# Performance work log

Measured on AMD Instinct MI355X. Metric: run time of the kernel, lower is better.

## Reference

```python
import jax, jax.numpy as jnp
import numpy as np

N = 384      # max_nodes
H = 256      # layers[0] == layers[1] == layers[2]
Z = 128      # dim_z
ED = 128     # edge_dim
AH = ED // 2 # attention hidden

# complete directed graph: combinations (i<j) then reversed pairs
_i, _j = np.triu_indices(N, k=1)
_SRC = jnp.asarray(np.concatenate([_i, _j]), dtype=jnp.int32)  # edge_index[0]
_DST = jnp.asarray(np.concatenate([_j, _i]), dtype=jnp.int32)  # edge_index[1]


def setup_inputs() -> dict:
    key = jax.random.key(0)
    ks = jax.random.split(key, 16)
    def p(k, shape, fan_in):
        return jax.random.normal(k, shape, dtype=jnp.float32) * (1.0 / np.sqrt(fan_in))
    return {
        "z": jax.random.normal(ks[0], (1, Z), dtype=jnp.float32),
        # GRU (torch layout: W_ih [3H, Z], W_hh [3H, H]; gate order r, z, n)
        "gru_Wih": p(ks[1], (3 * H, Z), Z),
        "gru_Whh": p(ks[2], (3 * H, H), H),
        "gru_bih": jnp.zeros((3 * H,), jnp.float32),
        "gru_bhh": jnp.zeros((3 * H,), jnp.float32),
        # edge_generator MLP: 2H -> 4H -> ED
        "eg_W1": p(ks[3], (2 * H, 4 * H), 2 * H), "eg_b1": jnp.zeros((4 * H,), jnp.float32),
        "eg_W2": p(ks[4], (4 * H, ED), 4 * H),   "eg_b2": jnp.zeros((ED,), jnp.float32),
        # attention MLPs: (ED+H) -> ED//2 -> 1
        "att0_W1": p(ks[5], (ED + H, AH), ED + H), "att0_b1": jnp.zeros((AH,), jnp.float32),
        "att0_W2": p(ks[6], (AH, 1), AH),           "att0_b2": jnp.zeros((1,), jnp.float32),
        "att1_W1": p(ks[7], (ED + H, AH), ED + H), "att1_b1": jnp.zeros((AH,), jnp.float32),
        "att1_W2": p(ks[8], (AH, 1), AH),           "att1_b2": jnp.zeros((1,), jnp.float32),
        # EdgeConv output linears: H -> H
        "conv0_W": p(ks[9], (H, H), H),  "conv0_b": jnp.zeros((H,), jnp.float32),
        "conv1_W": p(ks[10], (H, H), H), "conv1_b": jnp.zeros((H,), jnp.float32),
    }


def _forward(z, gru_Wih, gru_Whh, gru_bih, gru_bhh,
             eg_W1, eg_b1, eg_W2, eg_b2,
             att0_W1, att0_b1, att0_W2, att0_b2,
             att1_W1, att1_b1, att1_W2, att1_b2,
             conv0_W, conv0_b, conv1_W, conv1_b):
    # --- GRU node generation: input is the same latent z at every step ---
    gi = z[0] @ gru_Wih.T + gru_bih            # [3H], constant per step
    gir, giz, gin = jnp.split(gi, 3)
    def step(h, _):
        gh = h @ gru_Whh.T + gru_bhh
        ghr, ghz, ghn = jnp.split(gh, 3)
        r = jax.nn.sigmoid(gir + ghr)
        u = jax.nn.sigmoid(giz + ghz)
        n = jnp.tanh(gin + r * ghn)
        h2 = (1.0 - u) * n + u * h
        return h2, h2
    _, nodes = jax.lax.scan(step, jnp.zeros((H,), z.dtype), None, length=N)  # [N, H]

    # --- edge features over the complete directed graph ---
    pairs = jnp.concatenate([nodes[_SRC], nodes[_DST]], axis=-1)            # [E, 2H]
    edges = jax.nn.relu(pairs @ eg_W1 + eg_b1) @ eg_W2 + eg_b2              # [E, ED]

    # --- EdgeConv: gather src, attention MLP gate, scatter-sum, linear ---
    def conv(x, aW1, ab1, aW2, ab2, W, b):
        xs = x[_SRC]                                                        # [E, H]
        a_in = jnp.concatenate([edges, xs], axis=-1)                        # [E, ED+H]
        att = jax.nn.sigmoid(jax.nn.relu(a_in @ aW1 + ab1) @ aW2 + ab2)     # [E, 1]
        agg = jax.ops.segment_sum(att * xs, _DST, num_segments=N)           # [N, H]
        return agg @ W + b

    x = jax.nn.relu(conv(nodes, att0_W1, att0_b1, att0_W2, att0_b2, conv0_W, conv0_b))
    x = conv(x, att1_W1, att1_b1, att1_W2, att1_b2, conv1_W, conv1_b)
    return jnp.sum(x, axis=0)                                               # [H]


def reference(z, gru_Wih, gru_Whh, gru_bih, gru_bhh,
              eg_W1, eg_b1, eg_W2, eg_b2,
              att0_W1, att0_b1, att0_W2, att0_b2,
              att1_W1, att1_b1, att1_W2, att1_b2,
              conv0_W, conv0_b, conv1_W, conv1_b):
    return _forward(z, gru_Wih, gru_Whh, gru_bih, gru_bhh,
                    eg_W1, eg_b1, eg_W2, eg_b2,
                    att0_W1, att0_b1, att0_W2, att0_b2,
                    att1_W1, att1_b1, att1_W2, att1_b2,
                    conv0_W, conv0_b, conv1_W, conv1_b)
```

## Files before the change

### kernel.cpp

```cpp
#include <hip/hip_runtime.h>
#include <hip/hip_fp16.h>
#include <cstdint>

#define DEV static __device__ __forceinline__

typedef _Float16 h2v __attribute__((ext_vector_type(2)));
typedef _Float16 half8 __attribute__((ext_vector_type(8)));
typedef float float4v __attribute__((ext_vector_type(4)));

union U32H2 { uint32_t u; _Float16 f[2]; };

DEV uint32_t pack_f2(float a, float b) {
    auto p = __builtin_amdgcn_cvt_pkrtz(a, b);
    return __builtin_bit_cast(uint32_t, p);
}

DEV half8 bc8(uint4 v) { return __builtin_bit_cast(half8, v); }

DEV float sigmoidf_(float x) { return 1.0f / (1.0f + __expf(-x)); }
DEV float tanh_fast(float x) { float e = __expf(-2.0f*x); return (1.0f - e) / (1.0f + e); }

DEV void gl_lds16(const void* gsrc, void* ldst) {
    __builtin_amdgcn_global_load_lds(
        (const __attribute__((address_space(1))) uint32_t*)gsrc,
        (__attribute__((address_space(3))) uint32_t*)ldst, 16, 0, 0);
}

static const size_t OFF_W16T  = 0;
static const size_t OFF_GI    = 98304;
static const size_t OFF_CC    = 99072;
static const size_t OFF_BF    = 99200;
static const size_t OFF_NODES = 164736;
static const size_t OFF_PF    = 263040;
static const size_t OFF_QF    = 459648;
static const size_t OFF_R0    = 656256;
static const size_t OFF_R1    = 680832;
static const size_t OFF_TT    = 705408;
static const size_t OFF_ATT0  = 10142592;
static const size_t OFF_ATT1  = 10290048;
static const size_t OFF_AGG   = 10437504;
static const size_t OFF_X0    = 10535808;
static const size_t OFF_CS    = 10634112;
static const size_t OFF_V     = 10634496;
static const size_t WS_TOTAL  = 10634752;

__global__ void k_prep_w16(const float* __restrict__ Whh, uint32_t* __restrict__ WL) {
    int o4 = blockIdx.x * 256 + threadIdx.x;
    int c = o4 >> 9, t = o4 & 511;
    int rt = c >> 3, kt = c & 7;
    int lane = t & 63, wv = t >> 6;
    int m = (wv*6 + rt)*16 + (lane & 15);
    int k0 = kt*32 + (lane >> 4)*8;
    const float* src = Whh + m*256 + k0;
    uint4 o;
    o.x = pack_f2(src[0], src[1]);
    o.y = pack_f2(src[2], src[3]);
    o.z = pack_f2(src[4], src[5]);
    o.w = pack_f2(src[6], src[7]);
    ((uint4*)WL)[o4] = o;
}

__global__ void k_prep_gi(const float* __restrict__ z, const float* __restrict__ Wih,
                          const float* __restrict__ bih, float* __restrict__ gi) {
    int o = blockIdx.x * 256 + threadIdx.x;
    float acc = bih[o];
    for (int i = 0; i < 128; ++i) acc += Wih[o*128 + i] * z[i];
    gi[o] = acc;
}

__global__ void k_prep_cc(const float* __restrict__ eg_b2, const float* __restrict__ a0W1,
                          const float* __restrict__ a1W1, float* __restrict__ cc) {
    int t = threadIdx.x;
    const float* A = (t < 64) ? a0W1 : a1W1;
    int j = t & 63;
    float acc = 0.f;
    for (int i = 0; i < 128; ++i) acc += eg_b2[i] * A[i*64 + j];
    cc[t] = acc;
}

__global__ void k_prep_w2a(const float* __restrict__ eg_W2, const float* __restrict__ a0W1,
                           const float* __restrict__ a1W1, uint32_t* __restrict__ BF) {
    int idx = blockIdx.x * 256 + threadIdx.x;
    int k2 = idx >> 7, n = idx & 127;
    const float* A = (n < 64) ? (a0W1 + n) : (a1W1 + (n - 64));
    const float* w0 = eg_W2 + (2*k2) * 128;
    float a = 0.f, b = 0.f;
    for (int i = 0; i < 128; ++i) {
        float av = A[i*64];
        a += w0[i] * av;
        b += w0[128 + i] * av;
    }
    int kk = k2 >> 4, jgrp = (k2 >> 2) & 3, sub = k2 & 3;
    int lane = jgrp*16 + (n & 15), t = n >> 4;
    BF[((kk*8 + t)*64 + lane)*4 + sub] = pack_f2(a, b);
}

__global__ void __launch_bounds__(512, 2)
k_gru(const float* __restrict__ gi, const float* __restrict__ bhh,
      const uint32_t* __restrict__ WL, float* __restrict__ nodes) {
    int tid = threadIdx.x;
    int lane = tid & 63, wv = tid >> 6;
    __shared__ __align__(16) _Float16 hh16[256];
    __shared__ float ghs[768];

    uint4 w[48];
    const uint4* wl4 = (const uint4*)WL;
    #pragma unroll
    for (int c = 0; c < 48; ++c) w[c] = wl4[c*512 + tid];
    #pragma unroll
    for (int c = 0; c < 48; ++c)
        asm volatile("" : "+a"(w[c].x), "+a"(w[c].y), "+a"(w[c].z), "+a"(w[c].w));

    float gir = 0.f, giz = 0.f, gin = 0.f, bh0 = 0.f, bh1 = 0.f, bh2 = 0.f;
    if (tid < 256) {
        gir = gi[tid]; giz = gi[256 + tid]; gin = gi[512 + tid];
        bh0 = bhh[tid]; bh1 = bhh[256 + tid]; bh2 = bhh[512 + tid];
    }
    float h = 0.f;
    if (tid < 128) ((uint32_t*)hh16)[tid] = 0u;
    __syncthreads();

    int kq = lane >> 4;
    bool writer = (lane & 15) == 0;
    int rowbase = wv*6*16 + kq*4;

    for (int t = 0; t < 384; ++t) {
        float4v d[6];
        #pragma unroll
        for (int rt = 0; rt < 6; ++rt) d[rt] = 0.f;

        half8 bcur = bc8(*(const uint4*)(hh16 + 0*32 + kq*8));
        #pragma unroll
        for (int kt = 0; kt < 8; ++kt) {
            half8 bnext;
            if (kt < 7) bnext = bc8(*(const uint4*)(hh16 + (kt+1)*32 + kq*8));
            #pragma unroll
            for (int rt = 0; rt < 6; ++rt)
                d[rt] = __builtin_amdgcn_mfma_f32_16x16x32_f16(
                    bc8(w[rt*8 + kt]), bcur, d[rt], 0, 0, 0);
            bcur = bnext;
        }

        if (writer) {
            #pragma unroll
            for (int rt = 0; rt < 6; ++rt)
                *(float4v*)(ghs + rowbase + rt*16) = d[rt];
        }
        __syncthreads();
        if (tid < 256) {
            float a0 = ghs[tid]       + bh0;
            float a1 = ghs[256 + tid] + bh1;
            float a2 = ghs[512 + tid] + bh2;
            float rg = sigmoidf_(gir + a0);
            float u  = sigmoidf_(giz + a1);
            float n  = tanh_fast(gin + rg * a2);
            h = (1.f - u) * n + u * h;
            hh16[tid] = (_Float16)h;
            nodes[t*256 + tid] = h;
        }
        __syncthreads();
    }
}

__global__ void k_pq(const float* __restrict__ nodes, const float* __restrict__ eg_W1,
                     const float* __restrict__ eg_b1, const float* __restrict__ a0W1,
                     const float* __restrict__ a0b1, const float* __restrict__ cc,
                     uint32_t* __restrict__ PF, uint32_t* __restrict__ QF,
                     float* __restrict__ R0) {
    int tid = threadIdx.x;
    int s0 = blockIdx.x * 4;
    __shared__ float ns[4][256];
    #pragma unroll
    for (int q = 0; q < 4; ++q) ns[q][tid] = nodes[(s0+q)*256 + tid];
    __syncthreads();

    int k0 = tid * 4;
    float acc[4][4];
    #pragma unroll
    for (int q = 0; q < 4; ++q) { acc[q][0]=0;acc[q][1]=0;acc[q][2]=0;acc[q][3]=0; }
    for (int i = 0; i < 256; ++i) {
        float4 wv = *(const float4*)&eg_W1[i*1024 + k0];
        #pragma unroll
        for (int q = 0; q < 4; ++q) {
            float nv = ns[q][i];
            acc[q][0] += nv*wv.x; acc[q][1] += nv*wv.y;
            acc[q][2] += nv*wv.z; acc[q][3] += nv*wv.w;
        }
    }
    float4 bv = *(const float4*)&eg_b1[k0];
    {
        int kk = k0 >> 5;
        int lgrp = ((k0 >> 3) & 3) * 16;
        int sub = (k0 & 7) >> 1;
        #pragma unroll
        for (int q = 0; q < 4; ++q) {
            int s = s0 + q, g = s >> 4, srow = s & 15;
            uint2 pw;
            pw.x = pack_f2(acc[q][0] + bv.x, acc[q][1] + bv.y);
            pw.y = pack_f2(acc[q][2] + bv.z, acc[q][3] + bv.w);
            *(uint2*)(PF + (((g*32 + kk)*64 + lgrp + srow) << 2) + sub) = pw;
        }
    }

    #pragma unroll
    for (int q = 0; q < 4; ++q) { acc[q][0]=0;acc[q][1]=0;acc[q][2]=0;acc[q][3]=0; }
    for (int i = 0; i < 256; ++i) {
        float4 wv = *(const float4*)&eg_W1[(256+i)*1024 + k0];
        #pragma unroll
        for (int q = 0; q < 4; ++q) {
            float nv = ns[q][i];
            acc[q][0] += nv*wv.x; acc[q][1] += nv*wv.y;
            acc[q][2] += nv*wv.z; acc[q][3] += nv*wv.w;
        }
    }
    #pragma unroll
    for (int q = 0; q < 4; ++q) {
        uint2 pw;
        pw.x = pack_f2(acc[q][0], acc[q][1]);
        pw.y = pack_f2(acc[q][2], acc[q][3]);
        ((uint2*)QF)[(s0+q)*256 + tid] = pw;
    }

    int srow = tid >> 6, j = tid & 63;
    float racc = a0b1[j] + cc[j];
    for (int i = 0; i < 256; ++i) racc += ns[srow][i] * a0W1[(128+i)*64 + j];
    R0[(s0+srow)*64 + j] = racc;
}

__global__ void __launch_bounds__(256, 2)
k_phaseA_mfma(const uint32_t* __restrict__ PF, const uint32_t* __restrict__ QF,
              const uint32_t* __restrict__ BF, uint32_t* __restrict__ TT) {
    __shared__ __align__(16) char smem[69632];
    uint4* Qs4 = (uint4*)smem;
    uint4* Ps4 = (uint4*)(smem + 32768);
    uint4* Bs4 = (uint4*)(smem + 36864);

    int tid = threadIdx.x;
    int lane = tid & 63, wv = tid >> 6;
    int g = blockIdx.x, d0 = blockIdx.y * 16;

    {
        const char* src = (const char*)(QF + (size_t)d0 * 512);
        for (int off = wv*1024 + lane*16; off < 32768; off += 4096)
            gl_lds16(src + off, (char*)Qs4 + off);
    }

    float4v acc[4][8];
    #pragma unroll
    for (int t = 0; t < 4; ++t)
        #pragma unroll
        for (int n = 0; n < 8; ++n) acc[t][n] = 0.f;

    for (int c = 0; c < 8; ++c) {
        __syncthreads();
        {
            const char* psrc = (const char*)(PF + (size_t)(g*32 + c*4) * 256);
            for (int off = wv*1024 + lane*16; off < 4096; off += 4096)
                gl_lds16(psrc + off, (char*)Ps4 + off);
            const char* bsrc = (const char*)(BF + (size_t)c * 8192);
            for (int off = wv*1024 + lane*16; off < 32768; off += 4096)
                gl_lds16(bsrc + off, (char*)Bs4 + off);
        }
        __syncthreads();

        #pragma unroll
        for (int kkl = 0; kkl < 4; ++kkl) {
            int kkg = c*4 + kkl;
            half8 b[8];
            #pragma unroll
            for (int n = 0; n < 8; ++n) b[n] = bc8(Bs4[(kkl*8 + n)*64 + lane]);
            half8 p8 = bc8(Ps4[kkl*64 + lane]);
            #pragma unroll
            for (int t = 0; t < 4; ++t) {
                half8 q8 = bc8(Qs4[(wv*4 + t)*128 + kkg*4 + (lane >> 4)]);
                half8 x = p8 + q8;
                half8 z = 0;
                x = __builtin_elementwise_max(x, z);
                #pragma unroll
                for (int n = 0; n < 8; ++n)
                    acc[t][n] = __builtin_amdgcn_mfma_f32_16x16x32_f16(x, b[n], acc[t][n], 0, 0, 0);
            }
        }
    }

    _Float16* epi = (_Float16*)(smem + 36864);
    int cn = lane & 15, rhi = (lane >> 4) * 4;
    for (int half = 0; half < 2; ++half) {
        __syncthreads();
        #pragma unroll
        for (int t = 0; t < 4; ++t) {
            int dl = wv*4 + t;
            #pragma unroll
            for (int n = 0; n < 4; ++n) {
                int j = n*16 + cn;
                float4v v = acc[t][half*4 + n];
                #pragma unroll
                for (int r = 0; r < 4; ++r)
                    epi[((rhi + r)*16 + dl)*64 + j] = (_Float16)v[r];
            }
        }
        __syncthreads();
        int srow = tid >> 4, dl = tid & 15;
        const uint4* src = (const uint4*)(epi + tid*64);
        uint4* dst = (uint4*)(TT + ((size_t)((g*16 + srow)*384 + d0 + dl))*64 + half*32);
        #pragma unroll
        for (int q = 0; q < 8; ++q) dst[q] = src[q];
    }
}

__global__ void k_att(const uint32_t* __restrict__ TT, const float* __restrict__ R,
                      const float* __restrict__ w2, const float* __restrict__ b2,
                      int off, float* __restrict__ ATT) {
    int p = blockIdx.x * 256 + threadIdx.x;
    int s = p / 384, d = p - s * 384;
    __shared__ float w2s[64];
    if (threadIdx.x < 64) w2s[threadIdx.x] = w2[threadIdx.x];
    __syncthreads();
    const uint4* tp = (const uint4*)(TT + (size_t)p*64 + off);
    const float* rp = R + s*64;
    float logit = b2[0];
    #pragma unroll
    for (int m = 0; m < 8; ++m) {
        uint4 tv = tp[m];
        uint32_t us[4] = {tv.x, tv.y, tv.z, tv.w};
        #pragma unroll
        for (int q = 0; q < 4; ++q) {
            U32H2 c; c.u = us[q];
            int j = m*8 + q*2;
            float h0 = fmaxf((float)c.f[0] + rp[j],   0.f);
            float h1 = fmaxf((float)c.f[1] + rp[j+1], 0.f);
            logit += h0*w2s[j] + h1*w2s[j+1];
        }
    }
    float a = 1.f / (1.f + __expf(-logit));
    ATT[p] = (s == d) ? 0.f : a;
}

__global__ void __launch_bounds__(256)
k_agg(const float* __restrict__ ATT, const float* __restrict__ X,
      float* __restrict__ AGG) {
    int tid = threadIdx.x;
    int d0 = blockIdx.x * 16;
    __shared__ float att_s[16][17];
    float acc[16];
    #pragma unroll
    for (int dl = 0; dl < 16; ++dl) acc[dl] = 0.f;

    for (int s0 = 0; s0 < 384; s0 += 16) {
        __syncthreads();
        {
            int row = tid >> 4, col = tid & 15;
            att_s[row][col] = ATT[(s0 + row)*384 + d0 + col];
        }
        __syncthreads();
        #pragma unroll 4
        for (int ss = 0; ss < 16; ++ss) {
            float x = X[(s0 + ss)*256 + tid];
            #pragma unroll
            for (int dl = 0; dl < 16; ++dl) acc[dl] += att_s[ss][dl] * x;
        }
    }
    #pragma unroll
    for (int dl = 0; dl < 16; ++dl)
        AGG[(d0 + dl)*256 + tid] = acc[dl];
}

__global__ void k_x0r1(const float* __restrict__ AGG, const float* __restrict__ W,
                       const float* __restrict__ b, const float* __restrict__ a1W1,
                       const float* __restrict__ a1b1, const float* __restrict__ cc,
                       float* __restrict__ X0, float* __restrict__ R1) {
    int d = blockIdx.x, tid = threadIdx.x;
    __shared__ float ag[256];
    __shared__ float xs[256];
    ag[tid] = AGG[d*256 + tid];
    __syncthreads();
    float acc = b[tid];
    for (int i = 0; i < 256; ++i) acc += ag[i] * W[i*256 + tid];
    acc = fmaxf(acc, 0.f);
    X0[d*256 + tid] = acc;
    xs[tid] = acc;
    __syncthreads();
    if (tid < 64) {
        float r = a1b1[tid] + cc[64 + tid];
        for (int i = 0; i < 256; ++i) r += xs[i] * a1W1[(128+i)*64 + tid];
        R1[d*64 + tid] = r;
    }
}

__global__ void k_colsum(const float* __restrict__ ATT, float* __restrict__ CS) {
    int s = blockIdx.x, t = threadIdx.x;
    float acc = 0.f;
    for (int d = t; d < 384; d += 64) acc += ATT[s*384 + d];
    for (int o = 32; o > 0; o >>= 1) acc += __shfl_down(acc, o, 64);
    if (t == 0) CS[s] = acc;
}

__global__ void k_v(const float* __restrict__ CS, const float* __restrict__ X0,
                    float* __restrict__ V) {
    int tid = threadIdx.x;
    __shared__ float cs[384];
    for (int q = tid; q < 384; q += 256) cs[q] = CS[q];
    __syncthreads();
    float acc = 0.f;
    for (int s = 0; s < 384; s += 4) {
        acc += cs[s]*X0[s*256 + tid] + cs[s+1]*X0[(s+1)*256 + tid]
             + cs[s+2]*X0[(s+2)*256 + tid] + cs[s+3]*X0[(s+3)*256 + tid];
    }
    V[tid] = acc;
}

__global__ void k_out(const float* __restrict__ V, const float* __restrict__ W,
                      const float* __restrict__ b, float* __restrict__ out) {
    int tid = threadIdx.x;
    __shared__ float vs[256];
    vs[tid] = V[tid];
    __syncthreads();
    float acc = 384.f * b[tid];
    for (int i = 0; i < 256; ++i) acc += vs[i] * W[i*256 + tid];
    out[tid] = acc;
}

extern "C" void kernel_launch(void* const* d_in, const int* in_sizes, int n_in,
                              void* d_out, int out_size, void* d_ws, size_t ws_size,
                              hipStream_t stream) {
    if (ws_size < WS_TOTAL * sizeof(uint32_t)) return;

    const float* z    = (const float*)d_in[0];
    const float* Wih  = (const float*)d_in[1];
    const float* Whh  = (const float*)d_in[2];
    const float* bih  = (const float*)d_in[3];
    const float* bhh  = (const float*)d_in[4];
    const float* egW1 = (const float*)d_in[5];
    const float* egb1 = (const float*)d_in[6];
    const float* egW2 = (const float*)d_in[7];
    const float* egb2 = (const float*)d_in[8];
    const float* a0W1 = (const float*)d_in[9];
    const float* a0b1 = (const float*)d_in[10];
    const float* a0W2 = (const float*)d_in[11];
    const float* a0b2 = (const float*)d_in[12];
    const float* a1W1 = (const float*)d_in[13];
    const float* a1b1 = (const float*)d_in[14];
    const float* a1W2 = (const float*)d_in[15];
    const float* a1b2 = (const float*)d_in[16];
    const float* c0W  = (const float*)d_in[17];
    const float* c0b  = (const float*)d_in[18];
    const float* c1W  = (const float*)d_in[19];
    const float* c1b  = (const float*)d_in[20];

    uint32_t* ws   = (uint32_t*)d_ws;
    uint32_t* WL   = ws + OFF_W16T;
    float*    gi   = (float*)(ws + OFF_GI);
    float*    cc   = (float*)(ws + OFF_CC);
    uint32_t* BF   = ws + OFF_BF;
    float*    nodes= (float*)(ws + OFF_NODES);
    uint32_t* PF   = ws + OFF_PF;
    uint32_t* QF   = ws + OFF_QF;
    float*    R0   = (float*)(ws + OFF_R0);
    float*    R1   = (float*)(ws + OFF_R1);
    uint32_t* TT   = ws + OFF_TT;
    float*    ATT0 = (float*)(ws + OFF_ATT0);
    float*    ATT1 = (float*)(ws + OFF_ATT1);
    float*    AGG  = (float*)(ws + OFF_AGG);
    float*    X0   = (float*)(ws + OFF_X0);
    float*    CS   = (float*)(ws + OFF_CS);
    float*    V    = (float*)(ws + OFF_V);
    float*    out  = (float*)d_out;

    hipLaunchKernelGGL(k_prep_w16,    dim3(96),  dim3(256), 0, stream, Whh, WL);
    hipLaunchKernelGGL(k_prep_gi,     dim3(3),   dim3(256), 0, stream, z, Wih, bih, gi);
    hipLaunchKernelGGL(k_prep_cc,     dim3(1),   dim3(128), 0, stream, egb2, a0W1, a1W1, cc);
    hipLaunchKernelGGL(k_prep_w2a,    dim3(256), dim3(256), 0, stream, egW2, a0W1, a1W1, BF);
    hipLaunchKernelGGL(k_gru,         dim3(1),   dim3(512), 0, stream, gi, bhh, WL, nodes);
    hipLaunchKernelGGL(k_pq,          dim3(96),  dim3(256), 0, stream, nodes, egW1, egb1, a0W1, a0b1, cc, PF, QF, R0);
    hipLaunchKernelGGL(k_phaseA_mfma, dim3(24, 24), dim3(256), 0, stream, PF, QF, BF, TT);
    hipLaunchKernelGGL(k_att,         dim3(576), dim3(256), 0, stream, TT, R0, a0W2, a0b2, 0,  ATT0);
    hipLaunchKernelGGL(k_agg,         dim3(24),  dim3(256), 0, stream, ATT0, nodes, AGG);
    hipLaunchKernelGGL(k_x0r1,        dim3(384), dim3(256), 0, stream, AGG, c0W, c0b, a1W1, a1b1, cc, X0, R1);
    hipLaunchKernelGGL(k_att,         dim3(576), dim3(256), 0, stream, TT, R1, a1W2, a1b2, 32, ATT1);
    hipLaunchKernelGGL(k_colsum,      dim3(384), dim3(64),  0, stream, ATT1, CS);
    hipLaunchKernelGGL(k_v,           dim3(1),   dim3(256), 0, stream, CS, X0, V);
    hipLaunchKernelGGL(k_out,         dim3(1),   dim3(256), 0, stream, V, c1W, c1b, out);
}
```

Baseline: 795.8 us.

## Reorder GRU weight tiles so each wave computes its own gates and drop a barrier

```diff
diff --git a/kernel.cpp b/kernel.cpp
--- a/kernel.cpp
+++ b/kernel.cpp
@@ -47,11 +47,11 @@
 __global__ void k_prep_w16(const float* __restrict__ Whh, uint32_t* __restrict__ WL) {
     int o4 = blockIdx.x * 256 + threadIdx.x;
     int c = o4 >> 9, t = o4 & 511;
-    int rt = c >> 3, kt = c & 7;
+    int g = c / 24, gate = (c >> 3) % 3, kt = c & 7;
     int lane = t & 63, wv = t >> 6;
-    int m = (wv*6 + rt)*16 + (lane & 15);
+    int row = gate*256 + (wv + 8*g)*16 + (lane & 15);
     int k0 = kt*32 + (lane >> 4)*8;
-    const float* src = Whh + m*256 + k0;
+    const float* src = Whh + row*256 + k0;
     uint4 o;
     o.x = pack_f2(src[0], src[1]);
     o.y = pack_f2(src[2], src[3]);
@@ -99,9 +99,8 @@
 k_gru(const float* __restrict__ gi, const float* __restrict__ bhh,
       const uint32_t* __restrict__ WL, float* __restrict__ nodes) {
     int tid = threadIdx.x;
-    int lane = tid & 63, wv = tid >> 6;
-    __shared__ __align__(16) _Float16 hh16[256];
-    __shared__ float ghs[768];
+    int lane = tid & 63, wv = tid >> 6, quad = lane >> 4;
+    __shared__ __align__(16) _Float16 hbuf[2][256];
 
     uint4 w[48];
     const uint4* wl4 = (const uint4*)WL;
@@ -111,52 +110,66 @@
     for (int c = 0; c < 48; ++c)
         asm volatile("" : "+a"(w[c].x), "+a"(w[c].y), "+a"(w[c].z), "+a"(w[c].w));
 
-    float gir = 0.f, giz = 0.f, gin = 0.f, bh0 = 0.f, bh1 = 0.f, bh2 = 0.f;
-    if (tid < 256) {
-        gir = gi[tid]; giz = gi[256 + tid]; gin = gi[512 + tid];
-        bh0 = bhh[tid]; bh1 = bhh[256 + tid]; bh2 = bhh[512 + tid];
-    }
-    float h = 0.f;
-    if (tid < 128) ((uint32_t*)hh16)[tid] = 0u;
-    __syncthreads();
-
-    int kq = lane >> 4;
+    float cr[2][4], cz[2][4], gn[2][4], bn[2][4], h[2][4];
+    #pragma unroll
+    for (int g = 0; g < 2; ++g) {
+        int ub = (wv + 8*g)*16 + quad*4;
+        #pragma unroll
+        for (int rg = 0; rg < 4; ++rg) {
+            int u = ub + rg;
+            cr[g][rg] = gi[u]       + bhh[u];
+            cz[g][rg] = gi[256 + u] + bhh[256 + u];
+            gn[g][rg] = gi[512 + u];
+            bn[g][rg] = bhh[512 + u];
+            h[g][rg]  = 0.f;
+        }
+    }
+    if (tid < 128) ((uint32_t*)hbuf[0])[tid] = 0u;
+    __syncthreads();
+
     bool writer = (lane & 15) == 0;
-    int rowbase = wv*6*16 + kq*4;
 
     for (int t = 0; t < 384; ++t) {
-        float4v d[6];
-        #pragma unroll
-        for (int rt = 0; rt < 6; ++rt) d[rt] = 0.f;
-
-        half8 bcur = bc8(*(const uint4*)(hh16 + 0*32 + kq*8));
+        const _Float16* hr = hbuf[t & 1];
+        _Float16* hw = hbuf[(t + 1) & 1];
+
+        float4v dd[6];
+        #pragma unroll
+        for (int i = 0; i < 6; ++i) dd[i] = 0.f;
+
+        half8 bcur = bc8(*(const uint4*)(hr + quad*8));
         #pragma unroll
         for (int kt = 0; kt < 8; ++kt) {
-            half8 bnext;
-            if (kt < 7) bnext = bc8(*(const uint4*)(hh16 + (kt+1)*32 + kq*8));
-            #pragma unroll
-            for (int rt = 0; rt < 6; ++rt)
-                d[rt] = __builtin_amdgcn_mfma_f32_16x16x32_f16(
-                    bc8(w[rt*8 + kt]), bcur, d[rt], 0, 0, 0);
+            half8 bnext = bcur;
+            if (kt < 7) bnext = bc8(*(const uint4*)(hr + (kt+1)*32 + quad*8));
+            #pragma unroll
+            for (int i = 0; i < 6; ++i)
+                dd[i] = __builtin_amdgcn_mfma_f32_16x16x32_f16(
+                    bc8(w[i*8 + kt]), bcur, dd[i], 0, 0, 0);
             bcur = bnext;
         }
 
+        #pragma unroll
+        for (int g = 0; g < 2; ++g)
+            #pragma unroll
+            for (int rg = 0; rg < 4; ++rg) {
+                float rgate = sigmoidf_(cr[g][rg] + dd[g*3 + 0][rg]);
+                float ugate = sigmoidf_(cz[g][rg] + dd[g*3 + 1][rg]);
+                float ngate = tanh_fast(gn[g][rg] + rgate*(dd[g*3 + 2][rg] + bn[g][rg]));
+                h[g][rg] = (1.f - ugate)*ngate + ugate*h[g][rg];
+            }
+
         if (writer) {
             #pragma unroll
-            for (int rt = 0; rt < 6; ++rt)
-                *(float4v*)(ghs + rowbase + rt*16) = d[rt];
-        }
-        __syncthreads();
-        if (tid < 256) {
-            float a0 = ghs[tid]       + bh0;
-            float a1 = ghs[256 + tid] + bh1;
-            float a2 = ghs[512 + tid] + bh2;
-            float rg = sigmoidf_(gir + a0);
-            float u  = sigmoidf_(giz + a1);
-            float n  = tanh_fast(gin + rg * a2);
-            h = (1.f - u) * n + u * h;
-            hh16[tid] = (_Float16)h;
-            nodes[t*256 + tid] = h;
+            for (int g = 0; g < 2; ++g) {
+                int ub = (wv + 8*g)*16 + quad*4;
+                uint2 hp;
+                hp.x = pack_f2(h[g][0], h[g][1]);
+                hp.y = pack_f2(h[g][2], h[g][3]);
+                *(uint2*)(hw + ub) = hp;
+                float4v hv = {h[g][0], h[g][1], h[g][2], h[g][3]};
+                *(float4v*)(nodes + t*256 + ub) = hv;
+            }
         }
         __syncthreads();
     }
```

Measured after the change: 1.671 ms. 110% more time.
